# Optimization experiments

Hardware: AMD Instinct MI355X
Metric: run time of the kernel (lower is better)

## Reference

```python
import jax, jax.numpy as jnp
import numpy as np

N_NODES = 50000
N_EDGES = 1_600_000
IN_C, HID_C, OUT_C = 512, 256, 50
ALPHA = 0.1
NUM_LAYERS = 10


def setup_inputs() -> dict:
    key = jax.random.key(0)
    ks = jax.random.split(key, 8)
    x = jax.random.normal(ks[0], (N_NODES, IN_C), dtype=jnp.float32)
    edge_row = jax.random.randint(ks[1], (N_EDGES,), 0, N_NODES, dtype=jnp.int32)
    edge_col = jax.random.randint(ks[2], (N_EDGES,), 0, N_NODES, dtype=jnp.int32)
    edge_weight = jax.random.uniform(ks[3], (N_EDGES,), dtype=jnp.float32)
    s1 = 1.0 / np.sqrt(IN_C)
    s2 = 1.0 / np.sqrt(HID_C)
    W1 = jax.random.uniform(ks[4], (IN_C, HID_C), minval=-s1, maxval=s1, dtype=jnp.float32)
    b1 = jax.random.uniform(ks[5], (HID_C,), minval=-s1, maxval=s1, dtype=jnp.float32)
    W2 = jax.random.uniform(ks[6], (HID_C, OUT_C), minval=-s2, maxval=s2, dtype=jnp.float32)
    b2 = jax.random.uniform(ks[7], (OUT_C,), minval=-s2, maxval=s2, dtype=jnp.float32)
    return {"x": x, "edge_row": edge_row, "edge_col": edge_col,
            "edge_weight": edge_weight, "W1": W1, "b1": b1, "W2": W2, "b2": b2}


def reference(x, edge_row, edge_col, edge_weight, W1, b1, W2, b2):
    # MLP: Linear -> ReLU -> Linear (dropout inactive in eval, no batch norm)
    h = jax.nn.relu(x @ W1 + b1)          # [N, HID_C]
    h = h @ W2 + b2                        # [N, OUT_C]
    x0 = h

    def spmm(v):
        # out[i] = sum_{e: row[e]==i} w[e] * v[col[e]]
        msgs = v[edge_col] * edge_weight[:, None]   # [E, OUT_C]
        return jax.ops.segment_sum(msgs, edge_row, num_segments=N_NODES)

    def step(h, _):
        h = spmm(h) * (1.0 - ALPHA) + ALPHA * x0
        return h, None

    h, _ = jax.lax.scan(step, h, None, length=NUM_LAYERS)
    return jax.nn.log_softmax(h, axis=1)
```

## Files before the change

### kernel.cpp

```cpp
#include <hip/hip_runtime.h>
#include <cstddef>
#include <cstdint>
#include <math.h>

#define N_NODES 50000
#define N_EDGES 1600000
#define IN_C 512
#define HID_C 256
#define OUT_C 50
#define PAD_C 64
#define NUM_LAYERS 10
#define NBUCK 98
#define BSHIFT 9
#define BCAP 20480
#define PHB_CHUNK 8192
#define PHB_BLOCKS 196

typedef __attribute__((ext_vector_type(8))) short short8;
typedef __attribute__((ext_vector_type(4))) float floatx4;

__device__ inline unsigned short f2bf(float f) {
    unsigned int u = __float_as_uint(f);
    u += 0x7fffu + ((u >> 16) & 1u);
    return (unsigned short)(u >> 16);
}

__device__ inline unsigned cvtpk(float lo, float hi) {
    unsigned r;
    asm("v_cvt_pk_bf16_f32 %0, %1, %2" : "=v"(r) : "v"(lo), "v"(hi));
    return r;
}

__device__ inline short8 pack_bf16x8(float4 lo, float4 hi) {
    union { unsigned u[4]; short8 s; } r;
    r.u[0] = cvtpk(lo.x, lo.y);
    r.u[1] = cvtpk(lo.z, lo.w);
    r.u[2] = cvtpk(hi.x, hi.y);
    r.u[3] = cvtpk(hi.z, hi.w);
    return r.s;
}

#define ASYNC16(g, l)                                                     \
    __builtin_amdgcn_global_load_lds(                                     \
        (const __attribute__((address_space(1))) void*)(g),               \
        (__attribute__((address_space(3))) void*)(l), 16, 0, 0)

#define WAITCNT6() asm volatile("s_waitcnt vmcnt(6)" ::: "memory")
#define WAITCNT0() asm volatile("s_waitcnt vmcnt(0)" ::: "memory")
#define SBAR()     __builtin_amdgcn_s_barrier()

__global__ __launch_bounds__(256) void transpose_w1(const float* __restrict__ W1,
                                                    unsigned short* __restrict__ Wt) {
    __shared__ float tile[32][33];
    int bx = blockIdx.x;
    int by = blockIdx.y;
    int tx = threadIdx.x & 31, ty = threadIdx.x >> 5;
#pragma unroll
    for (int i = 0; i < 32; i += 8)
        tile[ty + i][tx] = W1[(bx * 32 + ty + i) * HID_C + by * 32 + tx];
    __syncthreads();
#pragma unroll
    for (int i = 0; i < 32; i += 8)
        Wt[(size_t)(by * 32 + ty + i) * IN_C + bx * 32 + tx] = f2bf(tile[tx][ty + i]);
}

__global__ void pad_w2(const float* __restrict__ W2, const float* __restrict__ b2,
                       unsigned short* __restrict__ Wpt, float* __restrict__ bp) {
    int idx = blockIdx.x * blockDim.x + threadIdx.x;
    if (idx < PAD_C * HID_C) {
        int n = idx >> 8, k = idx & 255;
        float v = (n < OUT_C) ? W2[k * OUT_C + n] : 0.f;
        Wpt[idx] = f2bf(v);
    }
    if (idx < PAD_C) bp[idx] = (idx < OUT_C) ? b2[idx] : 0.f;
}

__global__ __launch_bounds__(256) void gemm1_fused(const float* __restrict__ A,
                                                   const unsigned short* __restrict__ Wt,
                                                   const float* __restrict__ b1,
                                                   const unsigned short* __restrict__ Wpt,
                                                   const float* __restrict__ bp,
                                                   unsigned short* __restrict__ h0b) {
    __shared__ __align__(16) char smem[73728];
    float*          Ab[3] = {(float*)smem,
                             (float*)(smem + 24576),
                             (float*)(smem + 49152)};
    unsigned short* Bb[3] = {(unsigned short*)(smem + 8192),
                             (unsigned short*)(smem + 32768),
                             (unsigned short*)(smem + 57344)};
    unsigned short* Hs = (unsigned short*)smem;
    const int HS_LD = 264;

    const int tid  = threadIdx.x;
    const int wave = tid >> 6, lane = tid & 63;
    const int quad = lane >> 4, l16 = lane & 15;
    const int m0 = blockIdx.x * 64;
    const int wm = (wave >> 1) * 32;
    const int wn = (wave & 1) * 128;

    floatx4 acc[2][8];
#pragma unroll
    for (int i = 0; i < 2; ++i)
#pragma unroll
        for (int j = 0; j < 8; ++j) acc[i][j] = (floatx4){0.f, 0.f, 0.f, 0.f};

    auto stage = [&](int bi, int ks) {
        const int k0 = ks << 5;
#pragma unroll
        for (int j = 0; j < 2; ++j) {
            int slot = tid + j * 256;
            int r = slot >> 3, c = slot & 7;
            int gr = m0 + r;
            if (gr >= N_NODES) gr = N_NODES - 1;
            const float* src = A + (size_t)gr * IN_C + k0 + ((c ^ (r & 7)) << 2);
            ASYNC16(src, Ab[bi] + (slot << 2));
        }
#pragma unroll
        for (int j = 0; j < 4; ++j) {
            int slot = tid + j * 256;
            int n = slot >> 2, c = slot & 3;
            int cs = c ^ ((n >> 1) & 3);
            const unsigned short* src = Wt + (size_t)n * IN_C + k0 + (cs << 3);
            ASYNC16(src, Bb[bi] + (slot << 3));
        }
    };

    auto compute = [&](int bi) {
        const float* As_ = Ab[bi];
        const unsigned short* Bs_ = Bb[bi];
        short8 bfr[8], afr[2];
#pragma unroll
        for (int nt = 0; nt < 8; ++nt) {
            int n  = wn + nt * 16 + l16;
            int cq = quad ^ ((n >> 1) & 3);
            bfr[nt] = *(const short8*)&Bs_[(n << 5) + (cq << 3)];
        }
#pragma unroll
        for (int mt = 0; mt < 2; ++mt) {
            int r  = wm + mt * 16 + l16;
            int rx = r & 7;
            float4 lo = *(const float4*)&As_[(r << 5) + (((2 * quad)     ^ rx) << 2)];
            float4 hi = *(const float4*)&As_[(r << 5) + (((2 * quad + 1) ^ rx) << 2)];
            afr[mt] = pack_bf16x8(lo, hi);
        }
#pragma unroll
        for (int mt = 0; mt < 2; ++mt)
#pragma unroll
            for (int nt = 0; nt < 8; ++nt)
                acc[mt][nt] = __builtin_amdgcn_mfma_f32_16x16x32_bf16(afr[mt], bfr[nt],
                                                                      acc[mt][nt], 0, 0, 0);
    };

    stage(0, 0);
    stage(1, 1);
#pragma unroll
    for (int ks = 0; ks < 14; ++ks) {
        WAITCNT6();
        SBAR();
        stage((ks + 2) % 3, ks + 2);
        compute(ks % 3);
    }
    WAITCNT6(); SBAR(); compute(2);
    WAITCNT0(); SBAR(); compute(0);
    __syncthreads();

#pragma unroll
    for (int nt = 0; nt < 8; ++nt) {
        int n = wn + nt * 16 + l16;
        float bn = b1[n];
#pragma unroll
        for (int mt = 0; mt < 2; ++mt)
#pragma unroll
            for (int r = 0; r < 4; ++r) {
                float v = acc[mt][nt][r] + bn;
                v = v > 0.f ? v : 0.f;
                Hs[(wm + mt * 16 + quad * 4 + r) * HS_LD + n] = f2bf(v);
            }
    }
    __syncthreads();

    floatx4 acc2[4];
#pragma unroll
    for (int nt = 0; nt < 4; ++nt) acc2[nt] = (floatx4){0.f, 0.f, 0.f, 0.f};
    const int hrow = (wave << 4) + l16;
#pragma unroll
    for (int k2 = 0; k2 < 8; ++k2) {
        short8 haf = *(const short8*)&Hs[hrow * HS_LD + (k2 << 5) + (quad << 3)];
#pragma unroll
        for (int nt = 0; nt < 4; ++nt) {
            short8 bf = *(const short8*)&Wpt[(size_t)((nt << 4) + l16) * HID_C + (k2 << 5) + (quad << 3)];
            acc2[nt] = __builtin_amdgcn_mfma_f32_16x16x32_bf16(haf, bf, acc2[nt], 0, 0, 0);
        }
    }
#pragma unroll
    for (int nt = 0; nt < 4; ++nt) {
        int c = (nt << 4) + l16;
        float bn = bp[c];
#pragma unroll
        for (int r = 0; r < 4; ++r) {
            int row = m0 + (wave << 4) + (quad << 2) + r;
            if (row < N_NODES)
                h0b[(size_t)row * PAD_C + c] = f2bf(acc2[nt][r] + bn);
        }
    }
}

__global__ __launch_bounds__(256) void bucket_scatter(const int* __restrict__ erow,
                                                      const int* __restrict__ ecol,
                                                      const float* __restrict__ ew,
                                                      int* __restrict__ bfill,
                                                      uint2* __restrict__ buckets) {
    __shared__ int lcnt[NBUCK];
    __shared__ int lbase[NBUCK];
    const int t = threadIdx.x;
    for (int b = t; b < NBUCK; b += 256) lcnt[b] = 0;
    __syncthreads();
    const int e0 = blockIdx.x * PHB_CHUNK;
    const int e1 = min(e0 + PHB_CHUNK, N_EDGES);
    for (int e = e0 + t; e < e1; e += 256)
        atomicAdd(&lcnt[erow[e] >> BSHIFT], 1);
    __syncthreads();
    for (int b = t; b < NBUCK; b += 256) {
        lbase[b] = atomicAdd(&bfill[b], lcnt[b]);
        lcnt[b] = 0;
    }
    __syncthreads();
    for (int e = e0 + t; e < e1; e += 256) {
        int r = erow[e];
        int b = r >> BSHIFT;
        int o = atomicAdd(&lcnt[b], 1);
        int idx = lbase[b] + o;
        if (idx < BCAP) {
            unsigned packed = ((unsigned)(r - (b << BSHIFT)) << 17) | (unsigned)ecol[e];
            buckets[(size_t)b * BCAP + idx] = make_uint2(packed, __float_as_uint(ew[e]));
        }
    }
}

__global__ __launch_bounds__(128) void bucket_scan(const int* __restrict__ bfill,
                                                   int* __restrict__ bbase,
                                                   int* __restrict__ rowptr) {
    __shared__ int sd[128];
    int t = threadIdx.x;
    int v = (t < NBUCK) ? min(bfill[t], BCAP) : 0;
    sd[t] = v;
    __syncthreads();
    for (int off = 1; off < 128; off <<= 1) {
        int x = (t >= off) ? sd[t - off] : 0;
        __syncthreads();
        sd[t] += x;
        __syncthreads();
    }
    if (t < NBUCK) bbase[t] = sd[t] - v;
    if (t == NBUCK - 1) {
        bbase[NBUCK] = sd[t];
        rowptr[N_NODES] = sd[t];
    }
}

__global__ __launch_bounds__(256) void bucket_csr(const uint2* __restrict__ buckets,
                                                  const int* __restrict__ bfill,
                                                  const int* __restrict__ bbase,
                                                  int* __restrict__ rowptr,
                                                  uint2* __restrict__ edges) {
    __shared__ int hist[512];
    __shared__ int excl[512];
    __shared__ int psum[256];
    const int b = blockIdx.x;
    const int t = threadIdx.x;
    const int n = min(bfill[b], BCAP);
    const uint2* bk = buckets + (size_t)b * BCAP;

    hist[t] = 0; hist[t + 256] = 0;
    __syncthreads();
    for (int i = t; i < n; i += 256)
        atomicAdd(&hist[bk[i].x >> 17], 1);
    __syncthreads();
    int a0 = hist[2 * t], a1 = hist[2 * t + 1];
    psum[t] = a0 + a1;
    __syncthreads();
    for (int off = 1; off < 256; off <<= 1) {
        int x = (t >= off) ? psum[t - off] : 0;
        __syncthreads();
        psum[t] += x;
        __syncthreads();
    }
    int pe = psum[t] - (a0 + a1);
    excl[2 * t] = pe;
    excl[2 * t + 1] = pe + a0;
    __syncthreads();
    const int base = bbase[b];
#pragma unroll
    for (int k = 0; k < 2; ++k) {
        int lr = t + k * 256;
        int r = (b << BSHIFT) + lr;
        if (r < N_NODES) rowptr[r] = base + excl[lr];
    }
    hist[t] = 0; hist[t + 256] = 0;
    __syncthreads();
    for (int i = t; i < n; i += 256) {
        uint2 ed = bk[i];
        int lr = ed.x >> 17;
        int pos = base + excl[lr] + atomicAdd(&hist[lr], 1);
        edges[pos] = make_uint2(ed.x & 0x1FFFFu, ed.y);
    }
}

__device__ inline void edge_fma(float* acc, float wgt, uint4 hv) {
    acc[0] = fmaf(wgt, __uint_as_float(hv.x << 16),         acc[0]);
    acc[1] = fmaf(wgt, __uint_as_float(hv.x & 0xffff0000u), acc[1]);
    acc[2] = fmaf(wgt, __uint_as_float(hv.y << 16),         acc[2]);
    acc[3] = fmaf(wgt, __uint_as_float(hv.y & 0xffff0000u), acc[3]);
    acc[4] = fmaf(wgt, __uint_as_float(hv.z << 16),         acc[4]);
    acc[5] = fmaf(wgt, __uint_as_float(hv.z & 0xffff0000u), acc[5]);
    acc[6] = fmaf(wgt, __uint_as_float(hv.w << 16),         acc[6]);
    acc[7] = fmaf(wgt, __uint_as_float(hv.w & 0xffff0000u), acc[7]);
}

template <bool LAST>
__global__ __launch_bounds__(256, 8) void prop8(const int* __restrict__ rowptr,
                                                const uint2* __restrict__ edges,
                                                const unsigned short* __restrict__ hin,
                                                const unsigned short* __restrict__ h0b,
                                                unsigned short* __restrict__ hout_b,
                                                float* __restrict__ out_f) {
    int wid = (blockIdx.x * blockDim.x + threadIdx.x) >> 6;
    if (wid >= N_NODES) return;
    int lane = threadIdx.x & 63;
    int slot = lane >> 3;
    int lc   = lane & 7;
    int s = rowptr[wid], e = rowptr[wid + 1];

    float acc0[8], acc1[8];
#pragma unroll
    for (int k = 0; k < 8; ++k) { acc0[k] = 0.f; acc1[k] = 0.f; }

    int i = s;
    for (; i + 32 <= e; i += 32) {
        uint2 cw0 = edges[i + slot];
        uint2 cw1 = edges[i + 8 + slot];
        uint2 cw2 = edges[i + 16 + slot];
        uint2 cw3 = edges[i + 24 + slot];
        uint4 hv0 = *(const uint4*)((const char*)hin + ((size_t)cw0.x << 7) + lc * 16);
        uint4 hv1 = *(const uint4*)((const char*)hin + ((size_t)cw1.x << 7) + lc * 16);
        uint4 hv2 = *(const uint4*)((const char*)hin + ((size_t)cw2.x << 7) + lc * 16);
        uint4 hv3 = *(const uint4*)((const char*)hin + ((size_t)cw3.x << 7) + lc * 16);
        edge_fma(acc0, __uint_as_float(cw0.y), hv0);
        edge_fma(acc1, __uint_as_float(cw1.y), hv1);
        edge_fma(acc0, __uint_as_float(cw2.y), hv2);
        edge_fma(acc1, __uint_as_float(cw3.y), hv3);
    }
    for (; i + 16 <= e; i += 16) {
        uint2 cw0 = edges[i + slot];
        uint2 cw1 = edges[i + 8 + slot];
        uint4 hv0 = *(const uint4*)((const char*)hin + ((size_t)cw0.x << 7) + lc * 16);
        uint4 hv1 = *(const uint4*)((const char*)hin + ((size_t)cw1.x << 7) + lc * 16);
        edge_fma(acc0, __uint_as_float(cw0.y), hv0);
        edge_fma(acc1, __uint_as_float(cw1.y), hv1);
    }
    for (; i < e; i += 8) {
        int idx = i + slot;
        uint2 cw = (idx < e) ? edges[idx] : make_uint2(0u, 0u);
        float wgt = (idx < e) ? __uint_as_float(cw.y) : 0.f;
        uint4 hv = *(const uint4*)((const char*)hin + ((size_t)cw.x << 7) + lc * 16);
        edge_fma(acc0, wgt, hv);
    }

    float r[8];
#pragma unroll
    for (int k = 0; k < 8; ++k) {
        float v = acc0[k] + acc1[k];
        v += __shfl_xor(v, 8, 64);
        v += __shfl_xor(v, 16, 64);
        v += __shfl_xor(v, 32, 64);
        r[k] = v;
    }

    uint4 h0v = *(const uint4*)((const char*)h0b + ((size_t)wid << 7) + lc * 16);
    float h0e[8];
    h0e[0] = __uint_as_float(h0v.x << 16);
    h0e[1] = __uint_as_float(h0v.x & 0xffff0000u);
    h0e[2] = __uint_as_float(h0v.y << 16);
    h0e[3] = __uint_as_float(h0v.y & 0xffff0000u);
    h0e[4] = __uint_as_float(h0v.z << 16);
    h0e[5] = __uint_as_float(h0v.z & 0xffff0000u);
    h0e[6] = __uint_as_float(h0v.w << 16);
    h0e[7] = __uint_as_float(h0v.w & 0xffff0000u);
#pragma unroll
    for (int k = 0; k < 8; ++k) r[k] = 0.9f * r[k] + 0.1f * h0e[k];

    if (!LAST) {
        if (slot == 0) {
            uint4 u;
            u.x = ((unsigned)f2bf(r[1]) << 16) | f2bf(r[0]);
            u.y = ((unsigned)f2bf(r[3]) << 16) | f2bf(r[2]);
            u.z = ((unsigned)f2bf(r[5]) << 16) | f2bf(r[4]);
            u.w = ((unsigned)f2bf(r[7]) << 16) | f2bf(r[6]);
            *(uint4*)((char*)hout_b + ((size_t)wid << 7) + lc * 16) = u;
        }
    } else {
        int ch0 = lc * 8;
        float m = -INFINITY;
#pragma unroll
        for (int k = 0; k < 8; ++k) if (ch0 + k < OUT_C) m = fmaxf(m, r[k]);
        m = fmaxf(m, __shfl_xor(m, 1, 64));
        m = fmaxf(m, __shfl_xor(m, 2, 64));
        m = fmaxf(m, __shfl_xor(m, 4, 64));
        float ss = 0.f;
#pragma unroll
        for (int k = 0; k < 8; ++k) if (ch0 + k < OUT_C) ss += __expf(r[k] - m);
        ss += __shfl_xor(ss, 1, 64);
        ss += __shfl_xor(ss, 2, 64);
        ss += __shfl_xor(ss, 4, 64);
        float lse = __logf(ss);
        if (slot == 0) {
#pragma unroll
            for (int k = 0; k < 8; ++k)
                if (ch0 + k < OUT_C)
                    out_f[(size_t)wid * OUT_C + ch0 + k] = (r[k] - m) - lse;
        }
    }
}

extern "C" void kernel_launch(void* const* d_in, const int* in_sizes, int n_in,
                              void* d_out, int out_size, void* d_ws, size_t ws_size,
                              hipStream_t stream) {
    const float* x    = (const float*)d_in[0];
    const int*   erow = (const int*)d_in[1];
    const int*   ecol = (const int*)d_in[2];
    const float* ew   = (const float*)d_in[3];
    const float* W1   = (const float*)d_in[4];
    const float* b1   = (const float*)d_in[5];
    const float* W2   = (const float*)d_in[6];
    const float* b2   = (const float*)d_in[7];
    float* out = (float*)d_out;

    char* p = (char*)d_ws;
    auto alloc = [&](size_t bytes) {
        char* r = p;
        p += (bytes + 255) & ~(size_t)255;
        return r;
    };
    char*  scratch = alloc((size_t)NBUCK * BCAP * 8);
    unsigned short* h0b = (unsigned short*)alloc((size_t)N_NODES * PAD_C * 2);
    uint2* edges  = (uint2*)alloc((size_t)N_EDGES * 8);
    int*   rowptr = (int*)alloc((size_t)(N_NODES + 1) * 4);
    int*   bfill  = (int*)alloc((size_t)NBUCK * 4);
    int*   bbase  = (int*)alloc((size_t)(NBUCK + 1) * 4);
    float* bp     = (float*)alloc((size_t)PAD_C * 4);
    unsigned short* Wt  = (unsigned short*)alloc((size_t)HID_C * IN_C * 2);
    unsigned short* Wpt = (unsigned short*)alloc((size_t)PAD_C * HID_C * 2);
    uint2* buckets = (uint2*)scratch;
    unsigned short* ha = (unsigned short*)scratch;
    unsigned short* hb = (unsigned short*)(scratch + (size_t)N_NODES * PAD_C * 2);

    hipMemsetAsync(bfill, 0, (size_t)NBUCK * 4, stream);

    bucket_scatter<<<PHB_BLOCKS, 256, 0, stream>>>(erow, ecol, ew, bfill, buckets);
    bucket_scan<<<1, 128, 0, stream>>>(bfill, bbase, rowptr);
    bucket_csr<<<NBUCK, 256, 0, stream>>>(buckets, bfill, bbase, rowptr, edges);

    transpose_w1<<<dim3(IN_C / 32, HID_C / 32), 256, 0, stream>>>(W1, Wt);
    pad_w2<<<(PAD_C * HID_C + 255) / 256, 256, 0, stream>>>(W2, b2, Wpt, bp);
    gemm1_fused<<<(N_NODES + 63) / 64, 256, 0, stream>>>(x, Wt, b1, Wpt, bp, h0b);

    const int prop_blocks = (N_NODES * 64 + 255) / 256;
    const unsigned short* cur = h0b;
    unsigned short* nxt = ha;
    for (int l = 0; l < NUM_LAYERS - 1; ++l) {
        prop8<false><<<prop_blocks, 256, 0, stream>>>(rowptr, edges, cur, h0b,
                                                      nxt, nullptr);
        const unsigned short* t = nxt;
        nxt = (nxt == ha) ? hb : ha;
        cur = t;
    }
    prop8<true><<<prop_blocks, 256, 0, stream>>>(rowptr, edges, cur, h0b,
                                                 nullptr, out);
}
```

Measured before the change: 594.6 us.

## Fuse preprocessing kernels and overlap CSR build with MLP GEMM; nontemporal edge loads

Merges the bucket scatter, W1 transpose and W2 padding into one heterogeneous launch. It also merges the per-bucket CSR construction with the fused MLP GEMM into a single grid, where the first blocks build the CSR and the rest run the GEMM. This removes several kernel launches and lets the irregular CSR work run alongside the compute-bound GEMM. Separately, the propagation kernel now reads edge records as 64-bit nontemporal loads to keep the gathered feature rows in cache. The CSR blocks now carry the GEMM's large shared-memory allocation, and the nontemporal hint may alter caching behaviour.

```diff
diff --git a/kernel.cpp b/kernel.cpp
--- a/kernel.cpp
+++ b/kernel.cpp
@@ -15,6 +15,9 @@
 #define BCAP 20480
 #define PHB_CHUNK 8192
 #define PHB_BLOCKS 196
+#define TW_BLOCKS 128
+#define PW_BLOCKS 64
+#define GEMM_BLOCKS 782
 
 typedef __attribute__((ext_vector_type(8))) short short8;
 typedef __attribute__((ext_vector_type(4))) float floatx4;
@@ -49,191 +52,66 @@
 #define WAITCNT0() asm volatile("s_waitcnt vmcnt(0)" ::: "memory")
 #define SBAR()     __builtin_amdgcn_s_barrier()
 
-__global__ __launch_bounds__(256) void transpose_w1(const float* __restrict__ W1,
-                                                    unsigned short* __restrict__ Wt) {
+__global__ __launch_bounds__(256) void prep_fused(const int* __restrict__ erow,
+                                                  const int* __restrict__ ecol,
+                                                  const float* __restrict__ ew,
+                                                  int* __restrict__ bfill,
+                                                  uint2* __restrict__ buckets,
+                                                  const float* __restrict__ W1,
+                                                  unsigned short* __restrict__ Wt,
+                                                  const float* __restrict__ W2,
+                                                  const float* __restrict__ b2,
+                                                  unsigned short* __restrict__ Wpt,
+                                                  float* __restrict__ bp) {
+    __shared__ int  lcnt[NBUCK];
+    __shared__ int  lbase[NBUCK];
     __shared__ float tile[32][33];
-    int bx = blockIdx.x;
-    int by = blockIdx.y;
-    int tx = threadIdx.x & 31, ty = threadIdx.x >> 5;
-#pragma unroll
-    for (int i = 0; i < 32; i += 8)
-        tile[ty + i][tx] = W1[(bx * 32 + ty + i) * HID_C + by * 32 + tx];
-    __syncthreads();
-#pragma unroll
-    for (int i = 0; i < 32; i += 8)
-        Wt[(size_t)(by * 32 + ty + i) * IN_C + bx * 32 + tx] = f2bf(tile[tx][ty + i]);
-}
-
-__global__ void pad_w2(const float* __restrict__ W2, const float* __restrict__ b2,
-                       unsigned short* __restrict__ Wpt, float* __restrict__ bp) {
-    int idx = blockIdx.x * blockDim.x + threadIdx.x;
-    if (idx < PAD_C * HID_C) {
-        int n = idx >> 8, k = idx & 255;
-        float v = (n < OUT_C) ? W2[k * OUT_C + n] : 0.f;
-        Wpt[idx] = f2bf(v);
-    }
-    if (idx < PAD_C) bp[idx] = (idx < OUT_C) ? b2[idx] : 0.f;
-}
-
-__global__ __launch_bounds__(256) void gemm1_fused(const float* __restrict__ A,
-                                                   const unsigned short* __restrict__ Wt,
-                                                   const float* __restrict__ b1,
-                                                   const unsigned short* __restrict__ Wpt,
-                                                   const float* __restrict__ bp,
-                                                   unsigned short* __restrict__ h0b) {
-    __shared__ __align__(16) char smem[73728];
-    float*          Ab[3] = {(float*)smem,
-                             (float*)(smem + 24576),
-                             (float*)(smem + 49152)};
-    unsigned short* Bb[3] = {(unsigned short*)(smem + 8192),
-                             (unsigned short*)(smem + 32768),
-                             (unsigned short*)(smem + 57344)};
-    unsigned short* Hs = (unsigned short*)smem;
-    const int HS_LD = 264;
-
-    const int tid  = threadIdx.x;
-    const int wave = tid >> 6, lane = tid & 63;
-    const int quad = lane >> 4, l16 = lane & 15;
-    const int m0 = blockIdx.x * 64;
-    const int wm = (wave >> 1) * 32;
-    const int wn = (wave & 1) * 128;
-
-    floatx4 acc[2][8];
-#pragma unroll
-    for (int i = 0; i < 2; ++i)
-#pragma unroll
-        for (int j = 0; j < 8; ++j) acc[i][j] = (floatx4){0.f, 0.f, 0.f, 0.f};
-
-    auto stage = [&](int bi, int ks) {
-        const int k0 = ks << 5;
-#pragma unroll
-        for (int j = 0; j < 2; ++j) {
-            int slot = tid + j * 256;
-            int r = slot >> 3, c = slot & 7;
-            int gr = m0 + r;
-            if (gr >= N_NODES) gr = N_NODES - 1;
-            const float* src = A + (size_t)gr * IN_C + k0 + ((c ^ (r & 7)) << 2);
-            ASYNC16(src, Ab[bi] + (slot << 2));
-        }
-#pragma unroll
-        for (int j = 0; j < 4; ++j) {
-            int slot = tid + j * 256;
-            int n = slot >> 2, c = slot & 3;
-            int cs = c ^ ((n >> 1) & 3);
-            const unsigned short* src = Wt + (size_t)n * IN_C + k0 + (cs << 3);
-            ASYNC16(src, Bb[bi] + (slot << 3));
-        }
-    };
-
-    auto compute = [&](int bi) {
-        const float* As_ = Ab[bi];
-        const unsigned short* Bs_ = Bb[bi];
-        short8 bfr[8], afr[2];
-#pragma unroll
-        for (int nt = 0; nt < 8; ++nt) {
-            int n  = wn + nt * 16 + l16;
-            int cq = quad ^ ((n >> 1) & 3);
-            bfr[nt] = *(const short8*)&Bs_[(n << 5) + (cq << 3)];
-        }
-#pragma unroll
-        for (int mt = 0; mt < 2; ++mt) {
-            int r  = wm + mt * 16 + l16;
-            int rx = r & 7;
-            float4 lo = *(const float4*)&As_[(r << 5) + (((2 * quad)     ^ rx) << 2)];
-            float4 hi = *(const float4*)&As_[(r << 5) + (((2 * quad + 1) ^ rx) << 2)];
-            afr[mt] = pack_bf16x8(lo, hi);
-        }
-#pragma unroll
-        for (int mt = 0; mt < 2; ++mt)
-#pragma unroll
-            for (int nt = 0; nt < 8; ++nt)
-                acc[mt][nt] = __builtin_amdgcn_mfma_f32_16x16x32_bf16(afr[mt], bfr[nt],
-                                                                      acc[mt][nt], 0, 0, 0);
-    };
-
-    stage(0, 0);
-    stage(1, 1);
-#pragma unroll
-    for (int ks = 0; ks < 14; ++ks) {
-        WAITCNT6();
-        SBAR();
-        stage((ks + 2) % 3, ks + 2);
-        compute(ks % 3);
-    }
-    WAITCNT6(); SBAR(); compute(2);
-    WAITCNT0(); SBAR(); compute(0);
-    __syncthreads();
-
-#pragma unroll
-    for (int nt = 0; nt < 8; ++nt) {
-        int n = wn + nt * 16 + l16;
-        float bn = b1[n];
-#pragma unroll
-        for (int mt = 0; mt < 2; ++mt)
-#pragma unroll
-            for (int r = 0; r < 4; ++r) {
-                float v = acc[mt][nt][r] + bn;
-                v = v > 0.f ? v : 0.f;
-                Hs[(wm + mt * 16 + quad * 4 + r) * HS_LD + n] = f2bf(v);
+    const int bid = blockIdx.x;
+    const int t = threadIdx.x;
+
+    if (bid < PHB_BLOCKS) {
+        for (int b = t; b < NBUCK; b += 256) lcnt[b] = 0;
+        __syncthreads();
+        const int e0 = bid * PHB_CHUNK;
+        const int e1 = min(e0 + PHB_CHUNK, N_EDGES);
+        for (int e = e0 + t; e < e1; e += 256)
+            atomicAdd(&lcnt[erow[e] >> BSHIFT], 1);
+        __syncthreads();
+        for (int b = t; b < NBUCK; b += 256) {
+            lbase[b] = atomicAdd(&bfill[b], lcnt[b]);
+            lcnt[b] = 0;
+        }
+        __syncthreads();
+        for (int e = e0 + t; e < e1; e += 256) {
+            int r = erow[e];
+            int b = r >> BSHIFT;
+            int o = atomicAdd(&lcnt[b], 1);
+            int idx = lbase[b] + o;
+            if (idx < BCAP) {
+                unsigned packed = ((unsigned)(r - (b << BSHIFT)) << 17) | (unsigned)ecol[e];
+                buckets[(size_t)b * BCAP + idx] = make_uint2(packed, __float_as_uint(ew[e]));
             }
-    }
-    __syncthreads();
-
-    floatx4 acc2[4];
-#pragma unroll
-    for (int nt = 0; nt < 4; ++nt) acc2[nt] = (floatx4){0.f, 0.f, 0.f, 0.f};
-    const int hrow = (wave << 4) + l16;
-#pragma unroll
-    for (int k2 = 0; k2 < 8; ++k2) {
-        short8 haf = *(const short8*)&Hs[hrow * HS_LD + (k2 << 5) + (quad << 3)];
-#pragma unroll
-        for (int nt = 0; nt < 4; ++nt) {
-            short8 bf = *(const short8*)&Wpt[(size_t)((nt << 4) + l16) * HID_C + (k2 << 5) + (quad << 3)];
-            acc2[nt] = __builtin_amdgcn_mfma_f32_16x16x32_bf16(haf, bf, acc2[nt], 0, 0, 0);
-        }
-    }
-#pragma unroll
-    for (int nt = 0; nt < 4; ++nt) {
-        int c = (nt << 4) + l16;
-        float bn = bp[c];
-#pragma unroll
-        for (int r = 0; r < 4; ++r) {
-            int row = m0 + (wave << 4) + (quad << 2) + r;
-            if (row < N_NODES)
-                h0b[(size_t)row * PAD_C + c] = f2bf(acc2[nt][r] + bn);
-        }
-    }
-}
-
-__global__ __launch_bounds__(256) void bucket_scatter(const int* __restrict__ erow,
-                                                      const int* __restrict__ ecol,
-                                                      const float* __restrict__ ew,
-                                                      int* __restrict__ bfill,
-                                                      uint2* __restrict__ buckets) {
-    __shared__ int lcnt[NBUCK];
-    __shared__ int lbase[NBUCK];
-    const int t = threadIdx.x;
-    for (int b = t; b < NBUCK; b += 256) lcnt[b] = 0;
-    __syncthreads();
-    const int e0 = blockIdx.x * PHB_CHUNK;
-    const int e1 = min(e0 + PHB_CHUNK, N_EDGES);
-    for (int e = e0 + t; e < e1; e += 256)
-        atomicAdd(&lcnt[erow[e] >> BSHIFT], 1);
-    __syncthreads();
-    for (int b = t; b < NBUCK; b += 256) {
-        lbase[b] = atomicAdd(&bfill[b], lcnt[b]);
-        lcnt[b] = 0;
-    }
-    __syncthreads();
-    for (int e = e0 + t; e < e1; e += 256) {
-        int r = erow[e];
-        int b = r >> BSHIFT;
-        int o = atomicAdd(&lcnt[b], 1);
-        int idx = lbase[b] + o;
-        if (idx < BCAP) {
-            unsigned packed = ((unsigned)(r - (b << BSHIFT)) << 17) | (unsigned)ecol[e];
-            buckets[(size_t)b * BCAP + idx] = make_uint2(packed, __float_as_uint(ew[e]));
-        }
+        }
+    } else if (bid < PHB_BLOCKS + TW_BLOCKS) {
+        int tb = bid - PHB_BLOCKS;
+        int bx = tb & 15;
+        int by = tb >> 4;
+        int tx = t & 31, ty = t >> 5;
+#pragma unroll
+        for (int i = 0; i < 32; i += 8)
+            tile[ty + i][tx] = W1[(bx * 32 + ty + i) * HID_C + by * 32 + tx];
+        __syncthreads();
+#pragma unroll
+        for (int i = 0; i < 32; i += 8)
+            Wt[(size_t)(by * 32 + ty + i) * IN_C + bx * 32 + tx] = f2bf(tile[tx][ty + i]);
+    } else {
+        int idx = (bid - PHB_BLOCKS - TW_BLOCKS) * 256 + t;
+        if (idx < PAD_C * HID_C) {
+            int n = idx >> 8, k = idx & 255;
+            float v = (n < OUT_C) ? W2[k * OUT_C + n] : 0.f;
+            Wpt[idx] = f2bf(v);
+        }
+        if (idx < PAD_C) bp[idx] = (idx < OUT_C) ? b2[idx] : 0.f;
     }
 }
 
@@ -258,51 +136,181 @@
     }
 }
 
-__global__ __launch_bounds__(256) void bucket_csr(const uint2* __restrict__ buckets,
-                                                  const int* __restrict__ bfill,
-                                                  const int* __restrict__ bbase,
-                                                  int* __restrict__ rowptr,
-                                                  uint2* __restrict__ edges) {
-    __shared__ int hist[512];
-    __shared__ int excl[512];
-    __shared__ int psum[256];
-    const int b = blockIdx.x;
-    const int t = threadIdx.x;
-    const int n = min(bfill[b], BCAP);
-    const uint2* bk = buckets + (size_t)b * BCAP;
-
-    hist[t] = 0; hist[t + 256] = 0;
+__global__ __launch_bounds__(256) void csr_gemm_fused(
+        const uint2* __restrict__ buckets, const int* __restrict__ bfill,
+        const int* __restrict__ bbase, int* __restrict__ rowptr,
+        uint2* __restrict__ edges,
+        const float* __restrict__ A, const unsigned short* __restrict__ Wt,
+        const float* __restrict__ b1, const unsigned short* __restrict__ Wpt,
+        const float* __restrict__ bp, unsigned short* __restrict__ h0b) {
+    __shared__ __align__(16) char smem[73728];
+    const int bid = blockIdx.x;
+    const int tid = threadIdx.x;
+
+    if (bid < NBUCK) {
+        int* hist = (int*)smem;
+        int* excl = (int*)(smem + 2048);
+        int* psum = (int*)(smem + 4096);
+        const int b = bid;
+        const int t = tid;
+        const int n = min(bfill[b], BCAP);
+        const uint2* bk = buckets + (size_t)b * BCAP;
+
+        hist[t] = 0; hist[t + 256] = 0;
+        __syncthreads();
+        for (int i = t; i < n; i += 256)
+            atomicAdd(&hist[bk[i].x >> 17], 1);
+        __syncthreads();
+        int a0 = hist[2 * t], a1 = hist[2 * t + 1];
+        psum[t] = a0 + a1;
+        __syncthreads();
+        for (int off = 1; off < 256; off <<= 1) {
+            int x = (t >= off) ? psum[t - off] : 0;
+            __syncthreads();
+            psum[t] += x;
+            __syncthreads();
+        }
+        int pe = psum[t] - (a0 + a1);
+        excl[2 * t] = pe;
+        excl[2 * t + 1] = pe + a0;
+        __syncthreads();
+        const int base = bbase[b];
+#pragma unroll
+        for (int k = 0; k < 2; ++k) {
+            int lr = t + k * 256;
+            int r = (b << BSHIFT) + lr;
+            if (r < N_NODES) rowptr[r] = base + excl[lr];
+        }
+        hist[t] = 0; hist[t + 256] = 0;
+        __syncthreads();
+        for (int i = t; i < n; i += 256) {
+            uint2 ed = bk[i];
+            int lr = ed.x >> 17;
+            int pos = base + excl[lr] + atomicAdd(&hist[lr], 1);
+            edges[pos] = make_uint2(ed.x & 0x1FFFFu, ed.y);
+        }
+        return;
+    }
+
+    float*          Ab[3] = {(float*)smem,
+                             (float*)(smem + 24576),
+                             (float*)(smem + 49152)};
+    unsigned short* Bb[3] = {(unsigned short*)(smem + 8192),
+                             (unsigned short*)(smem + 32768),
+                             (unsigned short*)(smem + 57344)};
+    unsigned short* Hs = (unsigned short*)smem;
+    const int HS_LD = 264;
+
+    const int wave = tid >> 6, lane = tid & 63;
+    const int quad = lane >> 4, l16 = lane & 15;
+    const int m0 = (bid - NBUCK) * 64;
+    const int wm = (wave >> 1) * 32;
+    const int wn = (wave & 1) * 128;
+
+    floatx4 acc[2][8];
+#pragma unroll
+    for (int i = 0; i < 2; ++i)
+#pragma unroll
+        for (int j = 0; j < 8; ++j) acc[i][j] = (floatx4){0.f, 0.f, 0.f, 0.f};
+
+    auto stage = [&](int bi, int ks) {
+        const int k0 = ks << 5;
+#pragma unroll
+        for (int j = 0; j < 2; ++j) {
+            int slot = tid + j * 256;
+            int r = slot >> 3, c = slot & 7;
+            int gr = m0 + r;
+            if (gr >= N_NODES) gr = N_NODES - 1;
+            const float* src = A + (size_t)gr * IN_C + k0 + ((c ^ (r & 7)) << 2);
+            ASYNC16(src, Ab[bi] + (slot << 2));
+        }
+#pragma unroll
+        for (int j = 0; j < 4; ++j) {
+            int slot = tid + j * 256;
+            int n = slot >> 2, c = slot & 3;
+            int cs = c ^ ((n >> 1) & 3);
+            const unsigned short* src = Wt + (size_t)n * IN_C + k0 + (cs << 3);
+            ASYNC16(src, Bb[bi] + (slot << 3));
+        }
+    };
+
+    auto compute = [&](int bi) {
+        const float* As_ = Ab[bi];
+        const unsigned short* Bs_ = Bb[bi];
+        short8 bfr[8], afr[2];
+#pragma unroll
+        for (int nt = 0; nt < 8; ++nt) {
+            int n  = wn + nt * 16 + l16;
+            int cq = quad ^ ((n >> 1) & 3);
+            bfr[nt] = *(const short8*)&Bs_[(n << 5) + (cq << 3)];
+        }
+#pragma unroll
+        for (int mt = 0; mt < 2; ++mt) {
+            int r  = wm + mt * 16 + l16;
+            int rx = r & 7;
+            float4 lo = *(const float4*)&As_[(r << 5) + (((2 * quad)     ^ rx) << 2)];
+            float4 hi = *(const float4*)&As_[(r << 5) + (((2 * quad + 1) ^ rx) << 2)];
+            afr[mt] = pack_bf16x8(lo, hi);
+        }
+#pragma unroll
+        for (int mt = 0; mt < 2; ++mt)
+#pragma unroll
+            for (int nt = 0; nt < 8; ++nt)
+                acc[mt][nt] = __builtin_amdgcn_mfma_f32_16x16x32_bf16(afr[mt], bfr[nt],
+                                                                      acc[mt][nt], 0, 0, 0);
+    };
+
+    stage(0, 0);
+    stage(1, 1);
+#pragma unroll
+    for (int ks = 0; ks < 14; ++ks) {
+        WAITCNT6();
+        SBAR();
+        stage((ks + 2) % 3, ks + 2);
+        compute(ks % 3);
+    }
+    WAITCNT6(); SBAR(); compute(2);
+    WAITCNT0(); SBAR(); compute(0);
     __syncthreads();
-    for (int i = t; i < n; i += 256)
-        atomicAdd(&hist[bk[i].x >> 17], 1);
+
+#pragma unroll
+    for (int nt = 0; nt < 8; ++nt) {
+        int n = wn + nt * 16 + l16;
+        float bn = b1[n];
+#pragma unroll
+        for (int mt = 0; mt < 2; ++mt)
+#pragma unroll
+            for (int r = 0; r < 4; ++r) {
+                float v = acc[mt][nt][r] + bn;
+                v = v > 0.f ? v : 0.f;
+                Hs[(wm + mt * 16 + quad * 4 + r) * HS_LD + n] = f2bf(v);
+            }
+    }
     __syncthreads();
-    int a0 = hist[2 * t], a1 = hist[2 * t + 1];
-    psum[t] = a0 + a1;
-    __syncthreads();
-    for (int off = 1; off < 256; off <<= 1) {
-        int x = (t >= off) ? psum[t - off] : 0;
-        __syncthreads();
-        psum[t] += x;
-        __syncthreads();
-    }
-    int pe = psum[t] - (a0 + a1);
-    excl[2 * t] = pe;
-    excl[2 * t + 1] = pe + a0;
-    __syncthreads();
-    const int base = bbase[b];
-#pragma unroll
-    for (int k = 0; k < 2; ++k) {
-        int lr = t + k * 256;
-        int r = (b << BSHIFT) + lr;
-        if (r < N_NODES) rowptr[r] = base + excl[lr];
-    }
-    hist[t] = 0; hist[t + 256] = 0;
-    __syncthreads();
-    for (int i = t; i < n; i += 256) {
-        uint2 ed = bk[i];
-        int lr = ed.x >> 17;
-        int pos = base + excl[lr] + atomicAdd(&hist[lr], 1);
-        edges[pos] = make_uint2(ed.x & 0x1FFFFu, ed.y);
+
+    floatx4 acc2[4];
+#pragma unroll
+    for (int nt = 0; nt < 4; ++nt) acc2[nt] = (floatx4){0.f, 0.f, 0.f, 0.f};
+    const int hrow = (wave << 4) + l16;
+#pragma unroll
+    for (int k2 = 0; k2 < 8; ++k2) {
+        short8 haf = *(const short8*)&Hs[hrow * HS_LD + (k2 << 5) + (quad << 3)];
+#pragma unroll
+        for (int nt = 0; nt < 4; ++nt) {
+            short8 bf = *(const short8*)&Wpt[(size_t)((nt << 4) + l16) * HID_C + (k2 << 5) + (quad << 3)];
+            acc2[nt] = __builtin_amdgcn_mfma_f32_16x16x32_bf16(haf, bf, acc2[nt], 0, 0, 0);
+        }
+    }
+#pragma unroll
+    for (int nt = 0; nt < 4; ++nt) {
+        int c = (nt << 4) + l16;
+        float bn = bp[c];
+#pragma unroll
+        for (int r = 0; r < 4; ++r) {
+            int row = m0 + (wave << 4) + (quad << 2) + r;
+            if (row < N_NODES)
+                h0b[(size_t)row * PAD_C + c] = f2bf(acc2[nt][r] + bn);
+        }
     }
 }
 
@@ -330,6 +338,7 @@
     int slot = lane >> 3;
     int lc   = lane & 7;
     int s = rowptr[wid], e = rowptr[wid + 1];
+    const unsigned long long* e8 = (const unsigned long long*)edges;
 
     float acc0[8], acc1[8];
 #pragma unroll
@@ -337,32 +346,32 @@
 
     int i = s;
     for (; i + 32 <= e; i += 32) {
-        uint2 cw0 = edges[i + slot];
-        uint2 cw1 = edges[i + 8 + slot];
-        uint2 cw2 = edges[i + 16 + slot];
-        uint2 cw3 = edges[i + 24 + slot];
-        uint4 hv0 = *(const uint4*)((const char*)hin + ((size_t)cw0.x << 7) + lc * 16);
-        uint4 hv1 = *(const uint4*)((const char*)hin + ((size_t)cw1.x << 7) + lc * 16);
-        uint4 hv2 = *(const uint4*)((const char*)hin + ((size_t)cw2.x << 7) + lc * 16);
-        uint4 hv3 = *(const uint4*)((const char*)hin + ((size_t)cw3.x << 7) + lc * 16);
-        edge_fma(acc0, __uint_as_float(cw0.y), hv0);
-        edge_fma(acc1, __uint_as_float(cw1.y), hv1);
-        edge_fma(acc0, __uint_as_float(cw2.y), hv2);
-        edge_fma(acc1, __uint_as_float(cw3.y), hv3);
+        unsigned long long c0 = __builtin_nontemporal_load(e8 + i + slot);
+        unsigned long long c1 = __builtin_nontemporal_load(e8 + i + 8 + slot);
+        unsigned long long c2 = __builtin_nontemporal_load(e8 + i + 16 + slot);
+        unsigned long long c3 = __builtin_nontemporal_load(e8 + i + 24 + slot);
+        uint4 hv0 = *(const uint4*)((const char*)hin + (((size_t)(unsigned)c0) << 7) + lc * 16);
+        uint4 hv1 = *(const uint4*)((const char*)hin + (((size_t)(unsigned)c1) << 7) + lc * 16);
+        uint4 hv2 = *(const uint4*)((const char*)hin + (((size_t)(unsigned)c2) << 7) + lc * 16);
+        uint4 hv3 = *(const uint4*)((const char*)hin + (((size_t)(unsigned)c3) << 7) + lc * 16);
+        edge_fma(acc0, __uint_as_float((unsigned)(c0 >> 32)), hv0);
+        edge_fma(acc1, __uint_as_float((unsigned)(c1 >> 32)), hv1);
+        edge_fma(acc0, __uint_as_float((unsigned)(c2 >> 32)), hv2);
+        edge_fma(acc1, __uint_as_float((unsigned)(c3 >> 32)), hv3);
     }
     for (; i + 16 <= e; i += 16) {
-        uint2 cw0 = edges[i + slot];
-        uint2 cw1 = edges[i + 8 + slot];
-        uint4 hv0 = *(const uint4*)((const char*)hin + ((size_t)cw0.x << 7) + lc * 16);
-        uint4 hv1 = *(const uint4*)((const char*)hin + ((size_t)cw1.x << 7) + lc * 16);
-        edge_fma(acc0, __uint_as_float(cw0.y), hv0);
-        edge_fma(acc1, __uint_as_float(cw1.y), hv1);
+        unsigned long long c0 = __builtin_nontemporal_load(e8 + i + slot);
+        unsigned long long c1 = __builtin_nontemporal_load(e8 + i + 8 + slot);
+        uint4 hv0 = *(const uint4*)((const char*)hin + (((size_t)(unsigned)c0) << 7) + lc * 16);
+        uint4 hv1 = *(const uint4*)((const char*)hin + (((size_t)(unsigned)c1) << 7) + lc * 16);
+        edge_fma(acc0, __uint_as_float((unsigned)(c0 >> 32)), hv0);
+        edge_fma(acc1, __uint_as_float((unsigned)(c1 >> 32)), hv1);
     }
     for (; i < e; i += 8) {
         int idx = i + slot;
-        uint2 cw = (idx < e) ? edges[idx] : make_uint2(0u, 0u);
-        float wgt = (idx < e) ? __uint_as_float(cw.y) : 0.f;
-        uint4 hv = *(const uint4*)((const char*)hin + ((size_t)cw.x << 7) + lc * 16);
+        unsigned long long c0 = (idx < e) ? __builtin_nontemporal_load(e8 + idx) : 0ull;
+        float wgt = (idx < e) ? __uint_as_float((unsigned)(c0 >> 32)) : 0.f;
+        uint4 hv = *(const uint4*)((const char*)hin + (((size_t)(unsigned)c0) << 7) + lc * 16);
         edge_fma(acc0, wgt, hv);
     }
 
@@ -456,13 +465,14 @@
 
     hipMemsetAsync(bfill, 0, (size_t)NBUCK * 4, stream);
 
-    bucket_scatter<<<PHB_BLOCKS, 256, 0, stream>>>(erow, ecol, ew, bfill, buckets);
+    prep_fused<<<PHB_BLOCKS + TW_BLOCKS + PW_BLOCKS, 256, 0, stream>>>(
+        erow, ecol, ew, bfill, buckets, W1, Wt, W2, b2, Wpt, bp);
+
     bucket_scan<<<1, 128, 0, stream>>>(bfill, bbase, rowptr);
-    bucket_csr<<<NBUCK, 256, 0, stream>>>(buckets, bfill, bbase, rowptr, edges);
-
-    transpose_w1<<<dim3(IN_C / 32, HID_C / 32), 256, 0, stream>>>(W1, Wt);
-    pad_w2<<<(PAD_C * HID_C + 255) / 256, 256, 0, stream>>>(W2, b2, Wpt, bp);
-    gemm1_fused<<<(N_NODES + 63) / 64, 256, 0, stream>>>(x, Wt, b1, Wpt, bp, h0b);
+
+    csr_gemm_fused<<<NBUCK + GEMM_BLOCKS, 256, 0, stream>>>(
+        buckets, bfill, bbase, rowptr, edges,
+        x, Wt, b1, Wpt, bp, h0b);
 
     const int prop_blocks = (N_NODES * 64 + 255) / 256;
     const unsigned short* cur = h0b;
```

Result: slower. 613.6 us (+3.2%).
